# Optimization experiments

Measured on AMD Instinct MI355X. Metric: run time of the kernel, lower is better.

## Reference

```python
import jax, jax.numpy as jnp
import numpy as np

B, LQ, LA, H = 32, 1024, 1024, 512
NEG_INF = jnp.float32(-1e7)  # matches torch masked_fill_(-10000000.0)


def setup_inputs() -> dict:
    key = jax.random.key(0)
    k1, k2, k3, k4 = jax.random.split(key, 4)
    q = jax.random.normal(k1, (B, LQ, H), dtype=jnp.float32)
    a = jax.random.normal(k2, (B, LA, H), dtype=jnp.float32)
    q_mask = jax.random.randint(k3, (B, LQ, 1), 0, 2).astype(jnp.int32)
    a_mask = jax.random.randint(k4, (B, LA, 1), 0, 2).astype(jnp.int32)
    # learned scalar, initialized exactly as in __init__
    temperature = jnp.float32(1.0 / np.sqrt(H))
    return {"q": q, "a": a, "q_mask": q_mask, "a_mask": a_mask,
            "temperature": temperature}


def reference(q, a, q_mask, a_mask, temperature):
    # scaled co-attention scores: [B, Lq, La]
    attn = jnp.einsum('bqh,bah->bqa', q, a) * temperature
    # validity mask via outer product of per-token masks (nonzero = valid)
    mask = jnp.matmul(q_mask.astype(jnp.float32),
                      a_mask.transpose(0, 2, 1).astype(jnp.float32)) != 0
    attn = jnp.where(mask, attn, NEG_INF)
    # dual-axis softmax over the SAME score matrix
    attn_q = jax.nn.softmax(attn, axis=1)  # normalize over Lq
    attn_a = jax.nn.softmax(attn, axis=2)  # normalize over La
    # aggregation: a_s = attn_q^T @ q -> [B, La, H]; q_s = attn_a @ a -> [B, Lq, H]
    a_s = jnp.einsum('bqa,bqh->bah', attn_q, q)
    q_s = jnp.einsum('bqa,bah->bqh', attn_a, a)
    return (jnp.concatenate([q, q_s], axis=-1),
            jnp.concatenate([a, a_s], axis=-1))
```

## Files before the change

### kernel.cpp

```cpp
#include <hip/hip_runtime.h>
#include <cstdint>
#include <cstddef>

#define NB   32
#define LQA  1024
#define HD   512

typedef __attribute__((ext_vector_type(4))) float  f32x4;
typedef __attribute__((ext_vector_type(8))) short  s16x8;
typedef __attribute__((ext_vector_type(4))) unsigned short u16x4;

static __device__ __forceinline__ unsigned short f2bf(float f) {
  unsigned int u = __builtin_bit_cast(unsigned int, f);
  u += 0x7fffu + ((u >> 16) & 1u);
  return (unsigned short)(u >> 16);
}
static __device__ __forceinline__ float bf2f(unsigned short h) {
  unsigned int u = ((unsigned int)h) << 16;
  return __builtin_bit_cast(float, u);
}
static __device__ __forceinline__ u16x4 cvt4(f32x4 v) {
  u16x4 r;
  r.x = f2bf(v.x); r.y = f2bf(v.y); r.z = f2bf(v.z); r.w = f2bf(v.w);
  return r;
}

typedef __attribute__((address_space(1))) const void gas_void;
typedef __attribute__((address_space(3))) void las_void;
static __device__ __forceinline__ void gload_lds16(const void* g, void* l) {
  __builtin_amdgcn_global_load_lds((gas_void*)g, (las_void*)l, 16, 0, 0);
}

__global__ __launch_bounds__(256) void k_transpose_copy(
    const float* __restrict__ src,
    float* __restrict__ out_left,
    unsigned short* __restrict__ dstT,
    unsigned short* __restrict__ dstN)
{
  const int b  = blockIdx.z;
  const int h0 = blockIdx.x * 64;
  const int q0 = blockIdx.y * 64;
  const int t  = threadIdx.x;

  __shared__ unsigned short T[64 * 68];

  const float* sb = src + (size_t)b * LQA * HD;
  float* ob       = out_left + (size_t)b * LQA * 1024;
  unsigned short* db  = dstT + (size_t)b * HD * LQA;
  unsigned short* dbn = dstN + (size_t)b * LQA * HD;

#pragma unroll
  for (int j = 0; j < 4; ++j) {
    int f = t + 256 * j;
    int r = f >> 4;
    int c = (f & 15) * 4;
    f32x4 v = *(const f32x4*)(sb + (size_t)(q0 + r) * HD + h0 + c);
    *(f32x4*)(ob + (size_t)(q0 + r) * 1024 + h0 + c) = v;
    u16x4 cv = cvt4(v);
    *(u16x4*)&dbn[(size_t)(q0 + r) * HD + h0 + c] = cv;
    *(u16x4*)&T[r * 68 + c] = cv;
  }
  __syncthreads();
#pragma unroll
  for (int j = 0; j < 4; ++j) {
    int f = t + 256 * j;
    int orow = f >> 4;
    int c = (f & 15) * 4;
    u16x4 v;
    v.x = T[(c + 0) * 68 + orow];
    v.y = T[(c + 1) * 68 + orow];
    v.z = T[(c + 2) * 68 + orow];
    v.w = T[(c + 3) * 68 + orow];
    *(u16x4*)&db[(size_t)(h0 + orow) * LQA + q0 + c] = v;
  }
}

__global__ __launch_bounds__(256) void k_scores(
    const unsigned short* __restrict__ qb16, const unsigned short* __restrict__ ab16,
    const int* __restrict__ qmask, const int* __restrict__ amask,
    const float* __restrict__ temp_p,
    unsigned short* __restrict__ E, unsigned short* __restrict__ ET)
{
  const int b  = blockIdx.z;
  const int m0 = blockIdx.x * 128;
  const int n0 = blockIdx.y * 128;
  const int t  = threadIdx.x;
  const int lane = t & 63;
  const int w  = t >> 6;
  const int moff = (w & 1) * 64;
  const int noff = (w >> 1) * 64;
  const int lrow = lane & 15;
  const int quad = lane >> 4;

  __shared__ __align__(16) unsigned short smem[128 * 132];
  unsigned short* As = smem;
  unsigned short* Bs = smem + 4096;

  const unsigned short* qb = qb16 + (size_t)b * LQA * HD;
  const unsigned short* ab = ab16 + (size_t)b * LQA * HD;

  const int fa = t, fb = t + 256;
  const unsigned short* qg0 = qb + (size_t)(m0 + (fa >> 2)) * HD + (fa & 3) * 8;
  const unsigned short* qg1 = qb + (size_t)(m0 + (fb >> 2)) * HD + (fb & 3) * 8;
  const unsigned short* ag0 = ab + (size_t)(n0 + (fa >> 2)) * HD + (fa & 3) * 8;
  const unsigned short* ag1 = ab + (size_t)(n0 + (fb >> 2)) * HD + (fb & 3) * 8;
  unsigned short* As0 = As + w * 512;
  unsigned short* As1 = As + (4 + w) * 512;
  unsigned short* Bs0 = Bs + w * 512;
  unsigned short* Bs1 = Bs + (4 + w) * 512;

  f32x4 acc[4][4];
#pragma unroll
  for (int i = 0; i < 4; ++i)
#pragma unroll
    for (int j = 0; j < 4; ++j) acc[i][j] = (f32x4)0.f;

  for (int kt = 0; kt < HD / 32; ++kt) {
    const int ko = kt * 32;
    gload_lds16(qg0 + ko, As0);
    gload_lds16(qg1 + ko, As1);
    gload_lds16(ag0 + ko, Bs0);
    gload_lds16(ag1 + ko, Bs1);
    __syncthreads();
    s16x8 af[4], bfr[4];
#pragma unroll
    for (int i = 0; i < 4; ++i) {
      af[i]  = *(const s16x8*)&As[(moff + i * 16 + lrow) * 32 + quad * 8];
      bfr[i] = *(const s16x8*)&Bs[(noff + i * 16 + lrow) * 32 + quad * 8];
    }
#pragma unroll
    for (int i = 0; i < 4; ++i)
#pragma unroll
      for (int j = 0; j < 4; ++j)
        acc[i][j] = __builtin_amdgcn_mfma_f32_16x16x32_bf16(af[i], bfr[j], acc[i][j], 0, 0, 0);
    __syncthreads();
  }

  unsigned short* Cs = smem;
  const float temp = temp_p[0];
  const int* qmb = qmask + b * LQA;
  const int* amb = amask + b * LQA;
#pragma unroll
  for (int i = 0; i < 4; ++i) {
#pragma unroll
    for (int j = 0; j < 4; ++j) {
      int ncol = noff + j * 16 + lrow;
      float am = (amb[n0 + ncol] != 0) ? 1.f : 0.f;
#pragma unroll
      for (int r = 0; r < 4; ++r) {
        int mrow = moff + i * 16 + quad * 4 + r;
        float qm = (qmb[m0 + mrow] != 0) ? 1.f : 0.f;
        float e = __expf(acc[i][j][r] * temp) * am * qm;
        Cs[mrow * 132 + ncol] = f2bf(e);
      }
    }
  }
  __syncthreads();
  const size_t Ebase = (size_t)b * LQA * LQA;
#pragma unroll
  for (int jj = 0; jj < 16; ++jj) {
    int f = t + 256 * jj;
    int row = f >> 5;
    int c = (f & 31) * 4;
    u16x4 v = *(const u16x4*)&Cs[row * 132 + c];
    *(u16x4*)&E[Ebase + (size_t)(m0 + row) * LQA + n0 + c] = v;
  }
#pragma unroll
  for (int jj = 0; jj < 16; ++jj) {
    int f = t + 256 * jj;
    int orow = f >> 5;
    int c = (f & 31) * 4;
    u16x4 v;
    v.x = Cs[(c + 0) * 132 + orow];
    v.y = Cs[(c + 1) * 132 + orow];
    v.z = Cs[(c + 2) * 132 + orow];
    v.w = Cs[(c + 3) * 132 + orow];
    *(u16x4*)&ET[Ebase + (size_t)(n0 + orow) * LQA + m0 + c] = v;
  }
}

__global__ __launch_bounds__(256) void k_rowsum_stats(
    const unsigned short* __restrict__ Emat, float2* __restrict__ invadd)
{
  const int t = threadIdx.x;
  const int rowg = blockIdx.x * 16 + (t >> 4);
  const int s = t & 15;
  const unsigned short* rp = Emat + (size_t)rowg * LQA;
  float sum = 0.f;
#pragma unroll
  for (int it = 0; it < 16; ++it) {
    u16x4 v = *(const u16x4*)&rp[it * 64 + s * 4];
    sum += bf2f(v.x) + bf2f(v.y) + bf2f(v.z) + bf2f(v.w);
  }
  sum += __shfl_xor(sum, 1);
  sum += __shfl_xor(sum, 2);
  sum += __shfl_xor(sum, 4);
  sum += __shfl_xor(sum, 8);
  if (s == 0) {
    float2 o;
    if (sum > 0.f) { o.x = 1.f / sum; o.y = 0.f; }
    else           { o.x = 0.f;       o.y = 1.f / 1024.f; }
    invadd[rowg] = o;
  }
}

__global__ __launch_bounds__(256) void k_rowsum_plain(
    const unsigned short* __restrict__ M, float* __restrict__ sums)
{
  const int t = threadIdx.x;
  const int rowg = blockIdx.x * 16 + (t >> 4);
  const int s = t & 15;
  const unsigned short* rp = M + (size_t)rowg * LQA;
  float sum = 0.f;
#pragma unroll
  for (int it = 0; it < 16; ++it) {
    u16x4 v = *(const u16x4*)&rp[it * 64 + s * 4];
    sum += bf2f(v.x) + bf2f(v.y) + bf2f(v.z) + bf2f(v.w);
  }
  sum += __shfl_xor(sum, 1);
  sum += __shfl_xor(sum, 2);
  sum += __shfl_xor(sum, 4);
  sum += __shfl_xor(sum, 8);
  if (s == 0) sums[rowg] = sum;
}

__global__ __launch_bounds__(256) void k_agg(
    const unsigned short* __restrict__ Emat,
    const unsigned short* __restrict__ Bt,
    const float2* __restrict__ invadd,
    const float* __restrict__ bsum,
    float* __restrict__ outp)
{
  const int b  = blockIdx.z;
  const int m0 = blockIdx.x * 128;
  const int n0 = blockIdx.y * 128;
  const int t  = threadIdx.x;
  const int lane = t & 63;
  const int w  = t >> 6;
  const int moff = (w & 1) * 64;
  const int noff = (w >> 1) * 64;
  const int lrow = lane & 15;
  const int quad = lane >> 4;

  __shared__ __align__(16) unsigned short As[128 * 32];
  __shared__ __align__(16) unsigned short Bs[128 * 32];

  const unsigned short* Eb = Emat + (size_t)b * LQA * LQA;
  const unsigned short* Bb = Bt + (size_t)b * HD * LQA;

  const int fa = t, fb = t + 256;
  const unsigned short* eg0 = Eb + (size_t)(m0 + (fa >> 2)) * LQA + (fa & 3) * 8;
  const unsigned short* eg1 = Eb + (size_t)(m0 + (fb >> 2)) * LQA + (fb & 3) * 8;
  const unsigned short* bg0 = Bb + (size_t)(n0 + (fa >> 2)) * LQA + (fa & 3) * 8;
  const unsigned short* bg1 = Bb + (size_t)(n0 + (fb >> 2)) * LQA + (fb & 3) * 8;
  unsigned short* As0 = As + w * 512;
  unsigned short* As1 = As + (4 + w) * 512;
  unsigned short* Bs0 = Bs + w * 512;
  unsigned short* Bs1 = Bs + (4 + w) * 512;

  f32x4 acc[4][4];
#pragma unroll
  for (int i = 0; i < 4; ++i)
#pragma unroll
    for (int j = 0; j < 4; ++j) acc[i][j] = (f32x4)0.f;

  for (int kt = 0; kt < LQA / 32; ++kt) {
    const int ko = kt * 32;
    gload_lds16(eg0 + ko, As0);
    gload_lds16(eg1 + ko, As1);
    gload_lds16(bg0 + ko, Bs0);
    gload_lds16(bg1 + ko, Bs1);
    __syncthreads();
    s16x8 af[4], bfr[4];
#pragma unroll
    for (int i = 0; i < 4; ++i) {
      af[i]  = *(const s16x8*)&As[(moff + i * 16 + lrow) * 32 + quad * 8];
      bfr[i] = *(const s16x8*)&Bs[(noff + i * 16 + lrow) * 32 + quad * 8];
    }
#pragma unroll
    for (int i = 0; i < 4; ++i)
#pragma unroll
      for (int j = 0; j < 4; ++j)
        acc[i][j] = __builtin_amdgcn_mfma_f32_16x16x32_bf16(af[i], bfr[j], acc[i][j], 0, 0, 0);
    __syncthreads();
  }

  const float2* ia = invadd + b * LQA;
  const float* bs = bsum + b * HD;
  float* ob = outp + (size_t)b * LQA * 1024;
#pragma unroll
  for (int i = 0; i < 4; ++i) {
#pragma unroll
    for (int j = 0; j < 4; ++j) {
      int ncol = noff + j * 16 + lrow;
      float bsv = bs[n0 + ncol];
#pragma unroll
      for (int r = 0; r < 4; ++r) {
        int mrow = moff + i * 16 + quad * 4 + r;
        float2 v = ia[m0 + mrow];
        ob[(size_t)(m0 + mrow) * 1024 + 512 + n0 + ncol] =
            v.x * acc[i][j][r] + v.y * bsv;
      }
    }
  }
}

extern "C" void kernel_launch(void* const* d_in, const int* in_sizes, int n_in,
                              void* d_out, int out_size, void* d_ws, size_t ws_size,
                              hipStream_t stream) {
  (void)in_sizes; (void)n_in; (void)out_size; (void)ws_size;
  const float* q    = (const float*)d_in[0];
  const float* a    = (const float*)d_in[1];
  const int*   qm   = (const int*)d_in[2];
  const int*   am   = (const int*)d_in[3];
  const float* temp = (const float*)d_in[4];

  float* out0 = (float*)d_out;
  float* out1 = out0 + (size_t)NB * LQA * 1024;

  char* ws = (char*)d_ws;
  const size_t MB = 1024ull * 1024ull;
  unsigned short* E    = (unsigned short*)(ws);
  unsigned short* ET   = (unsigned short*)(ws + 64 * MB);
  unsigned short* qT   = (unsigned short*)(ws + 128 * MB);
  unsigned short* aT   = (unsigned short*)(ws + 160 * MB);
  unsigned short* qb16 = (unsigned short*)(ws + 192 * MB);
  unsigned short* ab16 = (unsigned short*)(ws + 224 * MB);
  float2* invq = (float2*)(ws + 256 * MB);
  float2* inva = (float2*)(ws + 256 * MB + 262144);
  float*  qsum = (float*)(ws + 256 * MB + 524288);
  float*  asum = (float*)(ws + 256 * MB + 524288 + 65536);

  k_transpose_copy<<<dim3(8, 16, NB), 256, 0, stream>>>(q, out0, qT, qb16);
  k_transpose_copy<<<dim3(8, 16, NB), 256, 0, stream>>>(a, out1, aT, ab16);
  k_rowsum_plain<<<dim3(NB * HD / 16), 256, 0, stream>>>(qT, qsum);
  k_rowsum_plain<<<dim3(NB * HD / 16), 256, 0, stream>>>(aT, asum);
  k_scores<<<dim3(8, 8, NB), 256, 0, stream>>>(qb16, ab16, qm, am, temp, E, ET);
  k_rowsum_stats<<<dim3(NB * LQA / 16), 256, 0, stream>>>(E, invq);
  k_rowsum_stats<<<dim3(NB * LQA / 16), 256, 0, stream>>>(ET, inva);
  k_agg<<<dim3(8, 4, NB), 256, 0, stream>>>(E,  aT, invq, asum, out0);
  k_agg<<<dim3(8, 4, NB), 256, 0, stream>>>(ET, qT, inva, qsum, out1);
}
```

Before: 628.4 us.

## Fuse row/column sums into score kernel via atomics and remap blocks per XCD

The score kernel now accumulates the bf16-rounded exp values into per-row and per-column partial sums, reduces them with wave shuffles, and atomically adds them to global buffers. This removes the two separate passes that re-read the 64MB E and ET matrices to compute sums. A small stats kernel turns the sums into inverse/add factors. The score and aggregation grids are also flattened and remapped so that all tiles of one batch land on the same XCD, which should improve L2 reuse. The cost is atomic traffic plus an extra memset.

Result: faster. 608.8 us (-3.1%).

```diff
diff --git a/kernel.cpp b/kernel.cpp
--- a/kernel.cpp
+++ b/kernel.cpp
@@ -79,11 +79,18 @@
     const unsigned short* __restrict__ qb16, const unsigned short* __restrict__ ab16,
     const int* __restrict__ qmask, const int* __restrict__ amask,
     const float* __restrict__ temp_p,
-    unsigned short* __restrict__ E, unsigned short* __restrict__ ET)
-{
-  const int b  = blockIdx.z;
-  const int m0 = blockIdx.x * 128;
-  const int n0 = blockIdx.y * 128;
+    unsigned short* __restrict__ E, unsigned short* __restrict__ ET,
+    float* __restrict__ rowsumE,
+    float* __restrict__ colsumE)
+{
+  const int flat = blockIdx.x;
+  const int xcd  = flat & 7;
+  const int i5   = flat >> 3;
+  const int b    = (i5 >> 6) * 8 + xcd;
+  const int tile = i5 & 63;
+  const int m0 = (tile & 7) * 128;
+  const int n0 = (tile >> 3) * 128;
+
   const int t  = threadIdx.x;
   const int lane = t & 63;
   const int w  = t >> 6;
@@ -140,6 +147,16 @@
   const float temp = temp_p[0];
   const int* qmb = qmask + b * LQA;
   const int* amb = amask + b * LQA;
+
+  float rowp[4][4];
+  float colp[4];
+#pragma unroll
+  for (int i = 0; i < 4; ++i)
+#pragma unroll
+    for (int r = 0; r < 4; ++r) rowp[i][r] = 0.f;
+#pragma unroll
+  for (int j = 0; j < 4; ++j) colp[j] = 0.f;
+
 #pragma unroll
   for (int i = 0; i < 4; ++i) {
 #pragma unroll
@@ -151,10 +168,33 @@
         int mrow = moff + i * 16 + quad * 4 + r;
         float qm = (qmb[m0 + mrow] != 0) ? 1.f : 0.f;
         float e = __expf(acc[i][j][r] * temp) * am * qm;
-        Cs[mrow * 132 + ncol] = f2bf(e);
+        unsigned short eb = f2bf(e);
+        float er = bf2f(eb);
+        Cs[mrow * 132 + ncol] = eb;
+        rowp[i][r] += er;
+        colp[j] += er;
       }
     }
   }
+
+#pragma unroll
+  for (int i = 0; i < 4; ++i)
+#pragma unroll
+    for (int r = 0; r < 4; ++r) {
+      float v = rowp[i][r];
+      v += __shfl_xor(v, 1); v += __shfl_xor(v, 2);
+      v += __shfl_xor(v, 4); v += __shfl_xor(v, 8);
+      if (lrow == 0)
+        atomicAdd(&rowsumE[(size_t)b * LQA + m0 + moff + i * 16 + quad * 4 + r], v);
+    }
+#pragma unroll
+  for (int j = 0; j < 4; ++j) {
+    float v = colp[j];
+    v += __shfl_xor(v, 16); v += __shfl_xor(v, 32);
+    if (quad == 0)
+      atomicAdd(&colsumE[(size_t)b * LQA + n0 + noff + j * 16 + lrow], v);
+  }
+
   __syncthreads();
   const size_t Ebase = (size_t)b * LQA * LQA;
 #pragma unroll
@@ -179,31 +219,6 @@
   }
 }
 
-__global__ __launch_bounds__(256) void k_rowsum_stats(
-    const unsigned short* __restrict__ Emat, float2* __restrict__ invadd)
-{
-  const int t = threadIdx.x;
-  const int rowg = blockIdx.x * 16 + (t >> 4);
-  const int s = t & 15;
-  const unsigned short* rp = Emat + (size_t)rowg * LQA;
-  float sum = 0.f;
-#pragma unroll
-  for (int it = 0; it < 16; ++it) {
-    u16x4 v = *(const u16x4*)&rp[it * 64 + s * 4];
-    sum += bf2f(v.x) + bf2f(v.y) + bf2f(v.z) + bf2f(v.w);
-  }
-  sum += __shfl_xor(sum, 1);
-  sum += __shfl_xor(sum, 2);
-  sum += __shfl_xor(sum, 4);
-  sum += __shfl_xor(sum, 8);
-  if (s == 0) {
-    float2 o;
-    if (sum > 0.f) { o.x = 1.f / sum; o.y = 0.f; }
-    else           { o.x = 0.f;       o.y = 1.f / 1024.f; }
-    invadd[rowg] = o;
-  }
-}
-
 __global__ __launch_bounds__(256) void k_rowsum_plain(
     const unsigned short* __restrict__ M, float* __restrict__ sums)
 {
@@ -222,6 +237,17 @@
   sum += __shfl_xor(sum, 4);
   sum += __shfl_xor(sum, 8);
   if (s == 0) sums[rowg] = sum;
+}
+
+__global__ __launch_bounds__(256) void k_stats(
+    const float* __restrict__ sums, float2* __restrict__ invadd)
+{
+  const int idx = blockIdx.x * 256 + threadIdx.x;
+  float s = sums[idx];
+  float2 o;
+  if (s > 0.f) { o.x = 1.f / s; o.y = 0.f; }
+  else         { o.x = 0.f;     o.y = 1.f / 1024.f; }
+  invadd[idx] = o;
 }
 
 __global__ __launch_bounds__(256) void k_agg(
@@ -231,9 +257,14 @@
     const float* __restrict__ bsum,
     float* __restrict__ outp)
 {
-  const int b  = blockIdx.z;
-  const int m0 = blockIdx.x * 128;
-  const int n0 = blockIdx.y * 128;
+  const int flat = blockIdx.x;
+  const int xcd  = flat & 7;
+  const int i5   = flat >> 3;
+  const int b    = (i5 >> 5) * 8 + xcd;
+  const int tile = i5 & 31;
+  const int m0 = (tile & 7) * 128;
+  const int n0 = (tile >> 3) * 128;
+
   const int t  = threadIdx.x;
   const int lane = t & 63;
   const int w  = t >> 6;
@@ -326,18 +357,19 @@
   unsigned short* aT   = (unsigned short*)(ws + 160 * MB);
   unsigned short* qb16 = (unsigned short*)(ws + 192 * MB);
   unsigned short* ab16 = (unsigned short*)(ws + 224 * MB);
-  float2* invq = (float2*)(ws + 256 * MB);
-  float2* inva = (float2*)(ws + 256 * MB + 262144);
-  float*  qsum = (float*)(ws + 256 * MB + 524288);
-  float*  asum = (float*)(ws + 256 * MB + 524288 + 65536);
+  float*  sums  = (float*)(ws + 256 * MB);
+  float2* invadd= (float2*)(ws + 256 * MB + (256 << 10));
+  float*  qsum  = (float*)(ws + 256 * MB + (768 << 10));
+  float*  asum  = (float*)(ws + 256 * MB + (832 << 10));
 
   k_transpose_copy<<<dim3(8, 16, NB), 256, 0, stream>>>(q, out0, qT, qb16);
   k_transpose_copy<<<dim3(8, 16, NB), 256, 0, stream>>>(a, out1, aT, ab16);
+  hipMemsetAsync(sums, 0, (size_t)2 * NB * LQA * sizeof(float), stream);
   k_rowsum_plain<<<dim3(NB * HD / 16), 256, 0, stream>>>(qT, qsum);
   k_rowsum_plain<<<dim3(NB * HD / 16), 256, 0, stream>>>(aT, asum);
-  k_scores<<<dim3(8, 8, NB), 256, 0, stream>>>(qb16, ab16, qm, am, temp, E, ET);
-  k_rowsum_stats<<<dim3(NB * LQA / 16), 256, 0, stream>>>(E, invq);
-  k_rowsum_stats<<<dim3(NB * LQA / 16), 256, 0, stream>>>(ET, inva);
-  k_agg<<<dim3(8, 4, NB), 256, 0, stream>>>(E,  aT, invq, asum, out0);
-  k_agg<<<dim3(8, 4, NB), 256, 0, stream>>>(ET, qT, inva, qsum, out1);
-}
+  k_scores<<<dim3(2048), 256, 0, stream>>>(qb16, ab16, qm, am, temp,
+                                           E, ET, sums, sums + NB * LQA);
+  k_stats<<<dim3(2 * NB * LQA / 256), 256, 0, stream>>>(sums, invadd);
+  k_agg<<<dim3(1024), 256, 0, stream>>>(E,  aT, invadd,            asum, out0);
+  k_agg<<<dim3(1024), 256, 0, stream>>>(ET, qT, invadd + NB * LQA, qsum, out1);
+}
```
